# Optimization experiments

Measured on AMD Instinct MI355X. Metric: run time of the kernel, lower is better.

The kernel has to match this reference:

```python
import jax, jax.numpy as jnp
import numpy as np

B, H, W, C = 8, 224, 224, 64
KH = KW = 3          # patch size
RANK = 100           # low rank
FILTERS = 256
IN_DIM = KH * KW * C  # 576


def extract_patches_same(x):
    """tf.image.extract_patches, sizes=3x3, strides=1, rates=1, SAME.

    Output channel ordering matches TF: [kh, kw, C] (spatial-major).
    x: (B,H,W,C) -> (B,H,W,KH*KW*C)
    """
    xp = jnp.pad(x, ((0, 0), (1, 1), (1, 1), (0, 0)))
    slices = [xp[:, di:di + H, dj:dj + W, :]
              for di in range(KH) for dj in range(KW)]
    return jnp.concatenate(slices, axis=-1)


def setup_inputs() -> dict:
    key = jax.random.key(0)
    ks = jax.random.split(key, 11)
    std = 0.05  # keras 'random_normal' initializer stddev
    return {
        "x": jax.random.normal(ks[0], (B, H, W, C), jnp.float32),
        "k": jax.random.normal(ks[1], (IN_DIM, RANK), jnp.float32) * std,
        "l_t": jax.random.normal(ks[2], (RANK, FILTERS), jnp.float32) * std,
        "s": jax.random.normal(ks[3], (RANK, RANK), jnp.float32) * std,
        "aux_U": jax.random.normal(ks[4], (IN_DIM, RANK), jnp.float32) * std,
        "aux_Unp1": jax.random.normal(ks[5], (IN_DIM, RANK), jnp.float32) * std,
        "aux_Vt": jax.random.normal(ks[6], (RANK, FILTERS), jnp.float32) * std,
        "aux_Vtnp1": jax.random.normal(ks[7], (RANK, FILTERS), jnp.float32) * std,
        "b": jax.random.normal(ks[8], (H, W, FILTERS), jnp.float32) * std,
        "aux_b": jax.random.normal(ks[9], (H, W, FILTERS), jnp.float32) * std,
        "step": 2,
    }


def reference(x, k, l_t, s, aux_U, aux_Unp1, aux_Vt, aux_Vtnp1, b, aux_b, step):
    patches = extract_patches_same(x)  # (B,H,W,IN_DIM)
    if step == 0:
        z = jnp.einsum('bhwp,pr->bhwr', patches, k)
        z = jnp.einsum('bhwr,rf->bhwf', z, aux_Vt) + aux_b
    elif step == 1:
        z = jnp.einsum('bhwp,pr->bhwr', patches, aux_U)
        z = jnp.einsum('bhwr,rf->bhwf', z, l_t) + aux_b
    else:
        z = jnp.einsum('bhwp,pr->bhwr', patches, aux_Unp1)
        z = jnp.einsum('bhwr,rq->bhwq', z, s)
        z = jnp.einsum('bhwq,qf->bhwf', z, aux_Vtnp1) + b
    return jax.nn.relu(z)
```

## Files before the change

kernel.cpp:

```cpp
#include <hip/hip_runtime.h>
#include <hip/hip_bf16.h>

#define H_ 224
#define W_ 224
#define C_ 64
#define F_ 256

typedef __attribute__((ext_vector_type(8))) short bf16x8;
typedef __attribute__((ext_vector_type(4))) float f32x4;

__device__ __forceinline__ unsigned short f2bf(float f) {
  union { float f; unsigned int u; } c; c.f = f;
  unsigned int u = c.u;
  return (unsigned short)((u + 0x7fffu + ((u >> 16) & 1u)) >> 16);
}

__global__ __launch_bounds__(256) void prep_kernel(
    const float* __restrict__ Unp1, const float* __restrict__ S,
    const float* __restrict__ Vt,
    unsigned short* __restrict__ uFrag, unsigned short* __restrict__ vFrag) {
  int u = blockIdx.x * 256 + threadIdx.x;
  if (u < 576 * 128) {
    int k = u >> 7;
    int n = u & 127;
    float acc = 0.f;
    if (n < 100) {
      for (int q = 0; q < 100; ++q)
        acc += Unp1[k * 100 + q] * S[q * 100 + n];
    }
    int ks = k >> 5, kk = k & 31, g = kk >> 3, j = kk & 7;
    int nt = n >> 4, lm = n & 15;
    uFrag[(((ks * 8 + nt) * 64) + g * 16 + lm) * 8 + j] = f2bf(acc);
  } else {
    int u2 = u - 576 * 128;
    if (u2 < 4 * 16 * 64 * 8) {
      int j = u2 & 7;
      int lane = (u2 >> 3) & 63;
      int nt = (u2 >> 9) & 15;
      int ks = u2 >> 13;
      int k = ks * 32 + (lane >> 4) * 8 + j;
      int n = nt * 16 + (lane & 15);
      float v = (k < 100) ? Vt[k * 256 + n] : 0.f;
      vFrag[u2] = f2bf(v);
    }
  }
}

__global__ __launch_bounds__(256, 4) void conv_kernel(
    const float* __restrict__ x,
    const unsigned short* __restrict__ uFrag,
    const unsigned short* __restrict__ vFrag,
    const float* __restrict__ bias,
    float* __restrict__ out) {
  __shared__ unsigned short xt[4 * 34 * 64];
  __shared__ unsigned short z1[64 * 128];

  int bid = blockIdx.x;
  int bb = bid & 7;
  int t2 = bid >> 3;
  int tw = t2 % 7;
  int th = t2 / 7;
  int h0 = th * 2, w0 = tw * 32;
  int tid = threadIdx.x;
  int lane = tid & 63, wid = tid >> 6;
  int wm = wid & 1, wn = wid >> 1;
  int g = lane >> 4, lm = lane & 15;

  const float* xb = x + (size_t)bb * (H_ * W_ * C_);
  #pragma unroll
  for (int it = 0; it < 5; ++it) {
    int i = tid + it * 256;
    if (i < 1088) {
      int row34 = i >> 3, c8 = i & 7;
      int r = row34 / 34;
      int ww = row34 - r * 34;
      int h = h0 - 1 + r, w = w0 - 1 + ww;
      bf16x8 sv;
      if (h >= 0 && h < H_ && w >= 0 && w < W_) {
        const float* p = xb + ((size_t)(h * W_ + w)) * C_ + c8 * 8;
        float4 f0 = *(const float4*)p;
        float4 f1 = *(const float4*)(p + 4);
        sv[0] = (short)f2bf(f0.x); sv[1] = (short)f2bf(f0.y);
        sv[2] = (short)f2bf(f0.z); sv[3] = (short)f2bf(f0.w);
        sv[4] = (short)f2bf(f1.x); sv[5] = (short)f2bf(f1.y);
        sv[6] = (short)f2bf(f1.z); sv[7] = (short)f2bf(f1.w);
      } else {
        sv = (bf16x8){0, 0, 0, 0, 0, 0, 0, 0};
      }
      *(bf16x8*)&xt[row34 * 64 + ((c8 ^ (row34 & 7)) << 3)] = sv;
    }
  }

  int rowoff[2][4];
  #pragma unroll
  for (int t = 0; t < 2; ++t) {
    #pragma unroll
    for (int i = 0; i < 4; ++i) {
      int mrow = (2 * wm + t) * 16 + g * 4 + i;
      int dh = mrow >> 5, dw = mrow & 31;
      rowoff[t][i] = (h0 + dh) * W_ + (w0 + dw);
    }
  }

  __syncthreads();

  float bv0[2][4][4];
  #pragma unroll
  for (int t = 0; t < 2; ++t)
    #pragma unroll
    for (int j = 0; j < 4; ++j)
      #pragma unroll
      for (int i = 0; i < 4; ++i)
        bv0[t][j][i] = bias[(size_t)rowoff[t][i] * F_ + (wn * 8 + j) * 16 + lm];

  f32x4 acc1[2][4] = {};
  #pragma unroll
  for (int ks = 0; ks < 18; ++ks) {
    int cell = ks >> 1;
    int kh = cell / 3, kw = cell - kh * 3;
    int c0c = (ks & 1) * 4;
    bf16x8 a[2];
    #pragma unroll
    for (int t = 0; t < 2; ++t) {
      int mrow = (2 * wm + t) * 16 + lm;
      int dh = mrow >> 5, dw = mrow & 31;
      int row34 = (dh + kh) * 34 + dw + kw;
      int chunk = (c0c + g) ^ (row34 & 7);
      a[t] = *(const bf16x8*)&xt[row34 * 64 + chunk * 8];
    }
    #pragma unroll
    for (int j = 0; j < 4; ++j) {
      int nt = wn * 4 + j;
      bf16x8 bq = *(const bf16x8*)&uFrag[(((ks * 8 + nt) * 64) + lane) * 8];
      acc1[0][j] = __builtin_amdgcn_mfma_f32_16x16x32_bf16(a[0], bq, acc1[0][j], 0, 0, 0);
      acc1[1][j] = __builtin_amdgcn_mfma_f32_16x16x32_bf16(a[1], bq, acc1[1][j], 0, 0, 0);
    }
  }

  #pragma unroll
  for (int t = 0; t < 2; ++t) {
    #pragma unroll
    for (int j = 0; j < 4; ++j) {
      int col = (wn * 4 + j) * 16 + lm;
      #pragma unroll
      for (int i = 0; i < 4; ++i) {
        int row = (2 * wm + t) * 16 + g * 4 + i;
        z1[row * 128 + (((col >> 3) ^ (row & 7)) << 3) + (col & 7)] = f2bf(acc1[t][j][i]);
      }
    }
  }
  __syncthreads();

  float bv1[2][4][4];
  #pragma unroll
  for (int t = 0; t < 2; ++t)
    #pragma unroll
    for (int j = 0; j < 4; ++j)
      #pragma unroll
      for (int i = 0; i < 4; ++i)
        bv1[t][j][i] = bias[(size_t)rowoff[t][i] * F_ + (wn * 8 + 4 + j) * 16 + lm];

  float* ob = out + (size_t)bb * (H_ * W_ * F_);

  {
    f32x4 acc2[2][4] = {};
    #pragma unroll
    for (int ks = 0; ks < 4; ++ks) {
      bf16x8 a[2];
      #pragma unroll
      for (int t = 0; t < 2; ++t) {
        int row = (2 * wm + t) * 16 + lm;
        int chunk = (ks * 4 + g) ^ (row & 7);
        a[t] = *(const bf16x8*)&z1[row * 128 + chunk * 8];
      }
      #pragma unroll
      for (int j = 0; j < 4; ++j) {
        int nt = wn * 8 + j;
        bf16x8 bq = *(const bf16x8*)&vFrag[(((ks * 16 + nt) * 64) + lane) * 8];
        acc2[0][j] = __builtin_amdgcn_mfma_f32_16x16x32_bf16(a[0], bq, acc2[0][j], 0, 0, 0);
        acc2[1][j] = __builtin_amdgcn_mfma_f32_16x16x32_bf16(a[1], bq, acc2[1][j], 0, 0, 0);
      }
    }
    #pragma unroll
    for (int t = 0; t < 2; ++t)
      #pragma unroll
      for (int j = 0; j < 4; ++j) {
        int f = (wn * 8 + j) * 16 + lm;
        #pragma unroll
        for (int i = 0; i < 4; ++i) {
          float v = fmaxf(acc2[t][j][i] + bv0[t][j][i], 0.f);
          __builtin_nontemporal_store(v, &ob[(size_t)rowoff[t][i] * F_ + f]);
        }
      }
  }

  {
    f32x4 acc2[2][4] = {};
    #pragma unroll
    for (int ks = 0; ks < 4; ++ks) {
      bf16x8 a[2];
      #pragma unroll
      for (int t = 0; t < 2; ++t) {
        int row = (2 * wm + t) * 16 + lm;
        int chunk = (ks * 4 + g) ^ (row & 7);
        a[t] = *(const bf16x8*)&z1[row * 128 + chunk * 8];
      }
      #pragma unroll
      for (int j = 0; j < 4; ++j) {
        int nt = wn * 8 + 4 + j;
        bf16x8 bq = *(const bf16x8*)&vFrag[(((ks * 16 + nt) * 64) + lane) * 8];
        acc2[0][j] = __builtin_amdgcn_mfma_f32_16x16x32_bf16(a[0], bq, acc2[0][j], 0, 0, 0);
        acc2[1][j] = __builtin_amdgcn_mfma_f32_16x16x32_bf16(a[1], bq, acc2[1][j], 0, 0, 0);
      }
    }
    #pragma unroll
    for (int t = 0; t < 2; ++t)
      #pragma unroll
      for (int j = 0; j < 4; ++j) {
        int f = (wn * 8 + 4 + j) * 16 + lm;
        #pragma unroll
        for (int i = 0; i < 4; ++i) {
          float v = fmaxf(acc2[t][j][i] + bv1[t][j][i], 0.f);
          __builtin_nontemporal_store(v, &ob[(size_t)rowoff[t][i] * F_ + f]);
        }
      }
  }
}

extern "C" void kernel_launch(void* const* d_in, const int* in_sizes, int n_in,
                              void* d_out, int out_size, void* d_ws, size_t ws_size,
                              hipStream_t stream) {
  const float* x     = (const float*)d_in[0];
  const float* S     = (const float*)d_in[3];
  const float* Unp1  = (const float*)d_in[5];
  const float* Vtnp1 = (const float*)d_in[7];
  const float* bias  = (const float*)d_in[8];
  float* out = (float*)d_out;

  unsigned short* uFrag = (unsigned short*)d_ws;
  unsigned short* vFrag = (unsigned short*)((char*)d_ws + 18 * 8 * 64 * 8 * 2);

  hipLaunchKernelGGL(prep_kernel, dim3(416), dim3(256), 0, stream,
                     Unp1, S, Vtnp1, uFrag, vFrag);
  hipLaunchKernelGGL(conv_kernel, dim3(8 * 112 * 7), dim3(256), 0, stream,
                     x, uFrag, vFrag, bias, out);
}
```

Measured before the change: 792.4 us.

## Split fused conv into two kernels to reuse bias across batch images

The fused kernel is split into a first GEMM kernel that writes the rank-100 intermediate (bf16, padded to 128) to a workspace buffer, and a second kernel that loads each pixel chunk's bias once and loops over all 8 images. The aim is to avoid re-reading the large per-pixel bias tensor for every batch image, and to keep the V fragments in registers. The cost is an extra round trip of about 100 MB of intermediate through global memory and one extra launch. The fused path is kept as a fallback when the workspace is too small.

```diff
diff --git a/kernel.cpp b/kernel.cpp
--- a/kernel.cpp
+++ b/kernel.cpp
@@ -5,6 +5,8 @@
 #define W_ 224
 #define C_ 64
 #define F_ 256
+#define NPIX 50176
+#define ZSTR 128
 
 typedef __attribute__((ext_vector_type(8))) short bf16x8;
 typedef __attribute__((ext_vector_type(4))) float f32x4;
@@ -46,20 +48,17 @@
   }
 }
 
-__global__ __launch_bounds__(256, 4) void conv_kernel(
+__global__ __launch_bounds__(256, 4) void g1_kernel(
     const float* __restrict__ x,
     const unsigned short* __restrict__ uFrag,
-    const unsigned short* __restrict__ vFrag,
-    const float* __restrict__ bias,
-    float* __restrict__ out) {
+    unsigned short* __restrict__ z) {
   __shared__ unsigned short xt[4 * 34 * 64];
   __shared__ unsigned short z1[64 * 128];
 
   int bid = blockIdx.x;
-  int bb = bid & 7;
-  int t2 = bid >> 3;
-  int tw = t2 % 7;
-  int th = t2 / 7;
+  int tw = bid % 7;
+  int th = (bid / 7) % 112;
+  int bb = bid / 784;
   int h0 = th * 2, w0 = tw * 32;
   int tid = threadIdx.x;
   int lane = tid & 63, wid = tid >> 6;
@@ -90,28 +89,7 @@
       *(bf16x8*)&xt[row34 * 64 + ((c8 ^ (row34 & 7)) << 3)] = sv;
     }
   }
-
-  int rowoff[2][4];
-  #pragma unroll
-  for (int t = 0; t < 2; ++t) {
-    #pragma unroll
-    for (int i = 0; i < 4; ++i) {
-      int mrow = (2 * wm + t) * 16 + g * 4 + i;
-      int dh = mrow >> 5, dw = mrow & 31;
-      rowoff[t][i] = (h0 + dh) * W_ + (w0 + dw);
-    }
-  }
-
   __syncthreads();
-
-  float bv0[2][4][4];
-  #pragma unroll
-  for (int t = 0; t < 2; ++t)
-    #pragma unroll
-    for (int j = 0; j < 4; ++j)
-      #pragma unroll
-      for (int i = 0; i < 4; ++i)
-        bv0[t][j][i] = bias[(size_t)rowoff[t][i] * F_ + (wn * 8 + j) * 16 + lm];
 
   f32x4 acc1[2][4] = {};
   #pragma unroll
@@ -151,6 +129,177 @@
   }
   __syncthreads();
 
+  #pragma unroll
+  for (int it = 0; it < 4; ++it) {
+    int i = tid + it * 256;
+    int row = i >> 4, c8 = i & 15;
+    bf16x8 v = *(const bf16x8*)&z1[row * 128 + ((c8 ^ (row & 7)) << 3)];
+    int pixel = (h0 + (row >> 5)) * W_ + w0 + (row & 31);
+    *(bf16x8*)&z[((size_t)bb * NPIX + pixel) * ZSTR + c8 * 8] = v;
+  }
+}
+
+__global__ __launch_bounds__(256, 2) void g2_kernel(
+    const unsigned short* __restrict__ z,
+    const unsigned short* __restrict__ vFrag,
+    const float* __restrict__ bias,
+    float* __restrict__ out) {
+  int chunk = blockIdx.x;
+  int tid = threadIdx.x;
+  int lane = tid & 63, w = tid >> 6;
+  int g = lane >> 4, lm = lane & 15;
+
+  bf16x8 B[4][4];
+  #pragma unroll
+  for (int ks = 0; ks < 4; ++ks)
+    #pragma unroll
+    for (int jn = 0; jn < 4; ++jn)
+      B[ks][jn] = *(const bf16x8*)&vFrag[(((ks * 16 + w * 4 + jn) * 64) + lane) * 8];
+
+  float bv[2][4][4];
+  #pragma unroll
+  for (int mt = 0; mt < 2; ++mt)
+    #pragma unroll
+    for (int jn = 0; jn < 4; ++jn)
+      #pragma unroll
+      for (int i = 0; i < 4; ++i) {
+        int px = chunk * 32 + mt * 16 + g * 4 + i;
+        bv[mt][jn][i] = bias[(size_t)px * F_ + (w * 4 + jn) * 16 + lm];
+      }
+
+  for (int img = 0; img < 8; ++img) {
+    const unsigned short* zb = z + ((size_t)img * NPIX + chunk * 32) * ZSTR;
+    bf16x8 A[2][4];
+    #pragma unroll
+    for (int mt = 0; mt < 2; ++mt)
+      #pragma unroll
+      for (int ks = 0; ks < 4; ++ks)
+        A[mt][ks] = *(const bf16x8*)&zb[(size_t)(mt * 16 + lm) * ZSTR + ks * 32 + g * 8];
+
+    f32x4 acc[2][4] = {};
+    #pragma unroll
+    for (int ks = 0; ks < 4; ++ks)
+      #pragma unroll
+      for (int jn = 0; jn < 4; ++jn) {
+        acc[0][jn] = __builtin_amdgcn_mfma_f32_16x16x32_bf16(A[0][ks], B[ks][jn], acc[0][jn], 0, 0, 0);
+        acc[1][jn] = __builtin_amdgcn_mfma_f32_16x16x32_bf16(A[1][ks], B[ks][jn], acc[1][jn], 0, 0, 0);
+      }
+
+    float* ob = out + ((size_t)img * NPIX + chunk * 32) * F_;
+    #pragma unroll
+    for (int mt = 0; mt < 2; ++mt)
+      #pragma unroll
+      for (int i = 0; i < 4; ++i) {
+        size_t pbase = (size_t)(mt * 16 + g * 4 + i) * F_;
+        #pragma unroll
+        for (int jn = 0; jn < 4; ++jn) {
+          float v = fmaxf(acc[mt][jn][i] + bv[mt][jn][i], 0.f);
+          ob[pbase + (w * 4 + jn) * 16 + lm] = v;
+        }
+      }
+  }
+}
+
+__global__ __launch_bounds__(256, 4) void fused_kernel(
+    const float* __restrict__ x,
+    const unsigned short* __restrict__ uFrag,
+    const unsigned short* __restrict__ vFrag,
+    const float* __restrict__ bias,
+    float* __restrict__ out) {
+  __shared__ unsigned short xt[4 * 34 * 64];
+  __shared__ unsigned short z1[64 * 128];
+
+  int bid = blockIdx.x;
+  int bb = bid & 7;
+  int t2 = bid >> 3;
+  int tw = t2 % 7;
+  int th = t2 / 7;
+  int h0 = th * 2, w0 = tw * 32;
+  int tid = threadIdx.x;
+  int lane = tid & 63, wid = tid >> 6;
+  int wm = wid & 1, wn = wid >> 1;
+  int g = lane >> 4, lm = lane & 15;
+
+  const float* xb = x + (size_t)bb * (H_ * W_ * C_);
+  #pragma unroll
+  for (int it = 0; it < 5; ++it) {
+    int i = tid + it * 256;
+    if (i < 1088) {
+      int row34 = i >> 3, c8 = i & 7;
+      int r = row34 / 34;
+      int ww = row34 - r * 34;
+      int h = h0 - 1 + r, w = w0 - 1 + ww;
+      bf16x8 sv;
+      if (h >= 0 && h < H_ && w >= 0 && w < W_) {
+        const float* p = xb + ((size_t)(h * W_ + w)) * C_ + c8 * 8;
+        float4 f0 = *(const float4*)p;
+        float4 f1 = *(const float4*)(p + 4);
+        sv[0] = (short)f2bf(f0.x); sv[1] = (short)f2bf(f0.y);
+        sv[2] = (short)f2bf(f0.z); sv[3] = (short)f2bf(f0.w);
+        sv[4] = (short)f2bf(f1.x); sv[5] = (short)f2bf(f1.y);
+        sv[6] = (short)f2bf(f1.z); sv[7] = (short)f2bf(f1.w);
+      } else {
+        sv = (bf16x8){0, 0, 0, 0, 0, 0, 0, 0};
+      }
+      *(bf16x8*)&xt[row34 * 64 + ((c8 ^ (row34 & 7)) << 3)] = sv;
+    }
+  }
+
+  int rowoff[2][4];
+  #pragma unroll
+  for (int t = 0; t < 2; ++t)
+    #pragma unroll
+    for (int i = 0; i < 4; ++i) {
+      int mrow = (2 * wm + t) * 16 + g * 4 + i;
+      rowoff[t][i] = (h0 + (mrow >> 5)) * W_ + (w0 + (mrow & 31));
+    }
+
+  __syncthreads();
+
+  float bv0[2][4][4];
+  #pragma unroll
+  for (int t = 0; t < 2; ++t)
+    #pragma unroll
+    for (int j = 0; j < 4; ++j)
+      #pragma unroll
+      for (int i = 0; i < 4; ++i)
+        bv0[t][j][i] = bias[(size_t)rowoff[t][i] * F_ + (wn * 8 + j) * 16 + lm];
+
+  f32x4 acc1[2][4] = {};
+  #pragma unroll
+  for (int ks = 0; ks < 18; ++ks) {
+    int cell = ks >> 1;
+    int kh = cell / 3, kw = cell - kh * 3;
+    int c0c = (ks & 1) * 4;
+    bf16x8 a[2];
+    #pragma unroll
+    for (int t = 0; t < 2; ++t) {
+      int mrow = (2 * wm + t) * 16 + lm;
+      int row34 = ((mrow >> 5) + kh) * 34 + (mrow & 31) + kw;
+      int chunk = (c0c + g) ^ (row34 & 7);
+      a[t] = *(const bf16x8*)&xt[row34 * 64 + chunk * 8];
+    }
+    #pragma unroll
+    for (int j = 0; j < 4; ++j) {
+      bf16x8 bq = *(const bf16x8*)&uFrag[(((ks * 8 + wn * 4 + j) * 64) + lane) * 8];
+      acc1[0][j] = __builtin_amdgcn_mfma_f32_16x16x32_bf16(a[0], bq, acc1[0][j], 0, 0, 0);
+      acc1[1][j] = __builtin_amdgcn_mfma_f32_16x16x32_bf16(a[1], bq, acc1[1][j], 0, 0, 0);
+    }
+  }
+
+  #pragma unroll
+  for (int t = 0; t < 2; ++t)
+    #pragma unroll
+    for (int j = 0; j < 4; ++j) {
+      int col = (wn * 4 + j) * 16 + lm;
+      #pragma unroll
+      for (int i = 0; i < 4; ++i) {
+        int row = (2 * wm + t) * 16 + g * 4 + i;
+        z1[row * 128 + (((col >> 3) ^ (row & 7)) << 3) + (col & 7)] = f2bf(acc1[t][j][i]);
+      }
+    }
+  __syncthreads();
+
   float bv1[2][4][4];
   #pragma unroll
   for (int t = 0; t < 2; ++t)
@@ -166,19 +315,18 @@
     f32x4 acc2[2][4] = {};
     #pragma unroll
     for (int ks = 0; ks < 4; ++ks) {
-      bf16x8 a[2];
+      bf16x8 a2[2];
       #pragma unroll
       for (int t = 0; t < 2; ++t) {
         int row = (2 * wm + t) * 16 + lm;
         int chunk = (ks * 4 + g) ^ (row & 7);
-        a[t] = *(const bf16x8*)&z1[row * 128 + chunk * 8];
+        a2[t] = *(const bf16x8*)&z1[row * 128 + chunk * 8];
       }
       #pragma unroll
       for (int j = 0; j < 4; ++j) {
-        int nt = wn * 8 + j;
-        bf16x8 bq = *(const bf16x8*)&vFrag[(((ks * 16 + nt) * 64) + lane) * 8];
-        acc2[0][j] = __builtin_amdgcn_mfma_f32_16x16x32_bf16(a[0], bq, acc2[0][j], 0, 0, 0);
-        acc2[1][j] = __builtin_amdgcn_mfma_f32_16x16x32_bf16(a[1], bq, acc2[1][j], 0, 0, 0);
+        bf16x8 bq = *(const bf16x8*)&vFrag[(((ks * 16 + wn * 8 + j) * 64) + lane) * 8];
+        acc2[0][j] = __builtin_amdgcn_mfma_f32_16x16x32_bf16(a2[0], bq, acc2[0][j], 0, 0, 0);
+        acc2[1][j] = __builtin_amdgcn_mfma_f32_16x16x32_bf16(a2[1], bq, acc2[1][j], 0, 0, 0);
       }
     }
     #pragma unroll
@@ -193,24 +341,22 @@
         }
       }
   }
-
   {
     f32x4 acc2[2][4] = {};
     #pragma unroll
     for (int ks = 0; ks < 4; ++ks) {
-      bf16x8 a[2];
+      bf16x8 a2[2];
       #pragma unroll
       for (int t = 0; t < 2; ++t) {
         int row = (2 * wm + t) * 16 + lm;
         int chunk = (ks * 4 + g) ^ (row & 7);
-        a[t] = *(const bf16x8*)&z1[row * 128 + chunk * 8];
+        a2[t] = *(const bf16x8*)&z1[row * 128 + chunk * 8];
       }
       #pragma unroll
       for (int j = 0; j < 4; ++j) {
-        int nt = wn * 8 + 4 + j;
-        bf16x8 bq = *(const bf16x8*)&vFrag[(((ks * 16 + nt) * 64) + lane) * 8];
-        acc2[0][j] = __builtin_amdgcn_mfma_f32_16x16x32_bf16(a[0], bq, acc2[0][j], 0, 0, 0);
-        acc2[1][j] = __builtin_amdgcn_mfma_f32_16x16x32_bf16(a[1], bq, acc2[1][j], 0, 0, 0);
+        bf16x8 bq = *(const bf16x8*)&vFrag[(((ks * 16 + wn * 8 + 4 + j) * 64) + lane) * 8];
+        acc2[0][j] = __builtin_amdgcn_mfma_f32_16x16x32_bf16(a2[0], bq, acc2[0][j], 0, 0, 0);
+        acc2[1][j] = __builtin_amdgcn_mfma_f32_16x16x32_bf16(a2[1], bq, acc2[1][j], 0, 0, 0);
       }
     }
     #pragma unroll
@@ -238,10 +384,19 @@
   float* out = (float*)d_out;
 
   unsigned short* uFrag = (unsigned short*)d_ws;
-  unsigned short* vFrag = (unsigned short*)((char*)d_ws + 18 * 8 * 64 * 8 * 2);
+  unsigned short* vFrag = (unsigned short*)((char*)d_ws + 147456);
+  unsigned short* zbuf  = (unsigned short*)((char*)d_ws + 212992);
+  const size_t NEED = 212992 + (size_t)8 * NPIX * ZSTR * 2;
 
   hipLaunchKernelGGL(prep_kernel, dim3(416), dim3(256), 0, stream,
                      Unp1, S, Vtnp1, uFrag, vFrag);
-  hipLaunchKernelGGL(conv_kernel, dim3(8 * 112 * 7), dim3(256), 0, stream,
-                     x, uFrag, vFrag, bias, out);
-}
+  if (ws_size >= NEED) {
+    hipLaunchKernelGGL(g1_kernel, dim3(8 * 112 * 7), dim3(256), 0, stream,
+                       x, uFrag, zbuf);
+    hipLaunchKernelGGL(g2_kernel, dim3(1568), dim3(256), 0, stream,
+                       zbuf, vFrag, bias, out);
+  } else {
+    hipLaunchKernelGGL(fused_kernel, dim3(8 * 112 * 7), dim3(256), 0, stream,
+                       x, uFrag, vFrag, bias, out);
+  }
+}
```

Result: faster. 735.8 us (-7.1%).
